# Optimization experiments

Hardware: AMD Instinct MI355X
Metric: run time of the kernel (lower is better)

The kernel has to match this reference:

```python
import jax, jax.numpy as jnp
import numpy as np

N, E, D, H, L = 50000, 800000, 256, 256, 40
HIDLAYERS = 3
NEG_SLOPE = 0.2  # PyG GATConv default leaky_relu slope


def _add_self_loops(edge_index, n):
    loop = jnp.arange(n, dtype=edge_index.dtype)
    src = jnp.concatenate([edge_index[0], loop])
    dst = jnp.concatenate([edge_index[1], loop])
    return src, dst


def gcn_conv(x, edge_index, W, b, n):
    # PyG GCNConv: add self-loops, symmetric deg^-1/2 normalization, linear, scatter-add
    src, dst = _add_self_loops(edge_index, n)
    ones = jnp.ones(src.shape[0], dtype=x.dtype)
    deg = jax.ops.segment_sum(ones, dst, num_segments=n)
    dinv = jnp.where(deg > 0, jax.lax.rsqrt(deg), 0.0)
    h = x @ W  # [n, out]
    norm = dinv[src] * dinv[dst]  # [E+n]
    out = jax.ops.segment_sum(h[src] * norm[:, None], dst, num_segments=n)
    return out + b


def gat_conv(x, edge_index, W, a_src, a_dst, b, n):
    # PyG GATConv (heads=1): add self-loops, e = leaky_relu(a_src.h_j + a_dst.h_i),
    # softmax over incoming edges per destination node, weighted scatter-add
    src, dst = _add_self_loops(edge_index, n)
    h = x @ W  # [n, H]
    al_src = h @ a_src  # [n]
    al_dst = h @ a_dst  # [n]
    e = jax.nn.leaky_relu(al_src[src] + al_dst[dst], NEG_SLOPE)  # [E+n]
    # numerically stable segment softmax over dst (self-loops => no empty segments)
    m = jax.ops.segment_max(e, dst, num_segments=n)
    ex = jnp.exp(e - m[dst])
    z = jax.ops.segment_sum(ex, dst, num_segments=n)
    alpha = ex / z[dst]
    out = jax.ops.segment_sum(h[src] * alpha[:, None], dst, num_segments=n)
    return out + b


def setup_inputs() -> dict:
    key = jax.random.key(0)
    ks = jax.random.split(key, 8)
    s = 0.05
    return {
        "x": jax.random.normal(ks[0], (N, D), jnp.float32),
        "edge_index": jax.random.randint(ks[1], (2, E), 0, N, dtype=jnp.int64),
        "W1": jax.random.normal(ks[2], (D, H), jnp.float32) * s,
        "b1": jnp.zeros((H,), jnp.float32),
        "Wg": jax.random.normal(ks[3], (H, H), jnp.float32) * s,
        "a_src": jax.random.normal(ks[4], (H,), jnp.float32) * s,
        "a_dst": jax.random.normal(ks[5], (H,), jnp.float32) * s,
        "bg": jnp.zeros((H,), jnp.float32),
        "W2": jax.random.normal(ks[6], (H, L), jnp.float32) * s,
        "b2": jnp.zeros((L,), jnp.float32),
    }


def reference(x, edge_index, W1, b1, Wg, a_src, a_dst, bg, W2, b2):
    n = x.shape[0]
    # feature standardization (torch .std is unbiased, ddof=1)
    x = (x - x.mean(axis=0, keepdims=True)) / x.std(axis=0, keepdims=True, ddof=1)
    x = jax.nn.relu(gcn_conv(x, edge_index, W1, b1, n))  # dropout = identity (eval)
    for _ in range(HIDLAYERS - 1):
        x = jax.nn.relu(gat_conv(x, edge_index, Wg, a_src, a_dst, bg, n))
    x = gcn_conv(x, edge_index, W2, b2, n)
    return jax.nn.log_softmax(x, axis=1)
```

## Files before the change

### kernel.cpp

```cpp
#include <hip/hip_runtime.h>
#include <math.h>

#define DD 256
#define LL 40
#define NSLOPE 0.2f
#define SCHUNK 1024

typedef unsigned short u16;
typedef unsigned int uint;
typedef __attribute__((ext_vector_type(8))) short short8;
typedef __attribute__((ext_vector_type(4))) float f32x4;

__device__ __forceinline__ float bf2f(u16 v) { return __uint_as_float(((uint)v) << 16); }
__device__ __forceinline__ u16 f2bf(float f) {
  uint u = __float_as_uint(f);
  return (u16)((u + 0x7fff + ((u >> 16) & 1)) >> 16);
}
__device__ __forceinline__ void acc8(float* a, uint4 v) {
  a[0] += __uint_as_float(v.x << 16);
  a[1] += __uint_as_float(v.x & 0xffff0000u);
  a[2] += __uint_as_float(v.y << 16);
  a[3] += __uint_as_float(v.y & 0xffff0000u);
  a[4] += __uint_as_float(v.z << 16);
  a[5] += __uint_as_float(v.z & 0xffff0000u);
  a[6] += __uint_as_float(v.w << 16);
  a[7] += __uint_as_float(v.w & 0xffff0000u);
}
__device__ __forceinline__ void wacc8(float* a, uint4 v, float w) {
  a[0] += w * __uint_as_float(v.x << 16);
  a[1] += w * __uint_as_float(v.x & 0xffff0000u);
  a[2] += w * __uint_as_float(v.y << 16);
  a[3] += w * __uint_as_float(v.y & 0xffff0000u);
  a[4] += w * __uint_as_float(v.z << 16);
  a[5] += w * __uint_as_float(v.z & 0xffff0000u);
  a[6] += w * __uint_as_float(v.w << 16);
  a[7] += w * __uint_as_float(v.w & 0xffff0000u);
}

__global__ void k_colstats(const float* __restrict__ x, float* __restrict__ csum,
                           float* __restrict__ csq, int n, int rowsPerBlk) {
  int col = threadIdx.x;
  int r0 = blockIdx.x * rowsPerBlk;
  int r1 = min(r0 + rowsPerBlk, n);
  float s = 0.f, q = 0.f;
  for (int r = r0; r < r1; ++r) {
    float v = x[(size_t)r * DD + col];
    s += v; q += v * v;
  }
  atomicAdd(&csum[col], s);
  atomicAdd(&csq[col], q);
}

__global__ void k_finalize_stats(const float* __restrict__ csum, const float* __restrict__ csq,
                                 float* __restrict__ mean, float* __restrict__ rstd, int n) {
  int j = threadIdx.x;
  float s = csum[j], q = csq[j];
  float m = s / (float)n;
  float var = (q - s * m) / (float)(n - 1);
  mean[j] = m;
  rstd[j] = 1.0f / sqrtf(var);
}

__global__ void k_standardize(const float* __restrict__ x, const float* __restrict__ mean,
                              const float* __restrict__ rstd, u16* __restrict__ xs, int total4) {
  int i = blockIdx.x * blockDim.x + threadIdx.x;
  if (i >= total4) return;
  int c4 = i & (DD / 4 - 1);
  float4 v = ((const float4*)x)[i];
  float4 m = ((const float4*)mean)[c4];
  float4 r = ((const float4*)rstd)[c4];
  uint2 o;
  o.x = (uint)f2bf((v.x - m.x) * r.x) | ((uint)f2bf((v.y - m.y) * r.y) << 16);
  o.y = (uint)f2bf((v.z - m.z) * r.z) | ((uint)f2bf((v.w - m.w) * r.w) << 16);
  ((uint2*)xs)[i] = o;
}

__global__ void k_convWt(const float* __restrict__ W, u16* __restrict__ Wt, int K, int N) {
  int k = blockIdx.x;
  for (int nn = threadIdx.x; nn < N; nn += blockDim.x)
    Wt[(size_t)nn * K + k] = f2bf(W[(size_t)k * N + nn]);
}

__global__ void k_count_deg(const int* __restrict__ edst, int E, int* __restrict__ degi) {
  int i = blockIdx.x * blockDim.x + threadIdx.x;
  if (i < E) atomicAdd(&degi[edst[i]], 1);
}

__global__ __launch_bounds__(256) void k_blocksum(const int* __restrict__ degi, int* __restrict__ bsum, int n) {
  int b = blockIdx.x, tid = threadIdx.x;
  int base = b * SCHUNK;
  int end = min(base + SCHUNK, n);
  int s = 0;
  for (int i = base + tid; i < end; i += 256) s += degi[i] + 1;
  __shared__ int ws[4];
  #pragma unroll
  for (int off = 32; off >= 1; off >>= 1) s += __shfl_down(s, off);
  if ((tid & 63) == 0) ws[tid >> 6] = s;
  __syncthreads();
  if (tid == 0) bsum[b] = ws[0] + ws[1] + ws[2] + ws[3];
}

__global__ void k_scan_bsums(int* __restrict__ bsum, int nb) {
  int lane = threadIdx.x;
  int orig = (lane < nb) ? bsum[lane] : 0;
  int v = orig;
  #pragma unroll
  for (int off = 1; off < 64; off <<= 1) {
    int t = __shfl_up(v, off);
    if (lane >= off) v += t;
  }
  if (lane < nb) bsum[lane] = v - orig;
}

__global__ __launch_bounds__(256) void k_rowptr_write(const int* __restrict__ degi, const int* __restrict__ bsum,
                                                      int* __restrict__ rowptr, int* __restrict__ cursor,
                                                      float* __restrict__ dinv, int n) {
  int b = blockIdx.x, tid = threadIdx.x;
  int base = b * SCHUNK + tid * 4;
  int d[4];
  int t = 0;
  #pragma unroll
  for (int j = 0; j < 4; ++j) {
    int i = base + j;
    d[j] = (i < n) ? degi[i] + 1 : 0;
    t += d[j];
  }
  __shared__ int sc[256];
  sc[tid] = t;
  __syncthreads();
  for (int off = 1; off < 256; off <<= 1) {
    int v = 0;
    if (tid >= off) v = sc[tid - off];
    __syncthreads();
    if (tid >= off) sc[tid] += v;
    __syncthreads();
  }
  int run = bsum[b] + sc[tid] - t;
  #pragma unroll
  for (int j = 0; j < 4; ++j) {
    int i = base + j;
    if (i < n) {
      rowptr[i] = run;
      cursor[i] = run;
      dinv[i] = rsqrtf((float)d[j]);
      run += d[j];
      if (i == n - 1) rowptr[n] = run;
    }
  }
}

__global__ void k_scatter(const int* __restrict__ esrc, const int* __restrict__ edst, int E,
                          int* __restrict__ cursor, int* __restrict__ csrsrc) {
  int i = blockIdx.x * blockDim.x + threadIdx.x;
  if (i < E) {
    int d = edst[i];
    int p = atomicAdd(&cursor[d], 1);
    csrsrc[p] = esrc[i];
  }
}

__global__ void k_selfloop(const int* __restrict__ rowptr, int* __restrict__ csrsrc, int n) {
  int i = blockIdx.x * blockDim.x + threadIdx.x;
  if (i < n) csrsrc[rowptr[i + 1] - 1] = i;
}

__global__ __launch_bounds__(256) void k_mfma_gemm(const u16* __restrict__ A, const u16* __restrict__ Bt,
                                                   u16* __restrict__ C, int M, int N, int K,
                                                   const float* __restrict__ rowScale) {
  __shared__ u16 As[128 * 40];
  __shared__ u16 Bs[64 * 40];
  int tid = threadIdx.x;
  int wave = tid >> 6, lane = tid & 63, quad = lane >> 4, l16 = lane & 15;
  int rowBase = blockIdx.y * 128, colBase = blockIdx.x * 64;
  f32x4 acc[2][4] = {};
  for (int k0 = 0; k0 < K; k0 += 32) {
    #pragma unroll
    for (int i = 0; i < 2; ++i) {
      int ch = tid + i * 256;
      int r = ch >> 2, cc = (ch & 3) * 8;
      int gr = rowBase + r;
      uint4 v = make_uint4(0, 0, 0, 0);
      if (gr < M) v = *(const uint4*)(A + (size_t)gr * K + k0 + cc);
      *(uint4*)&As[r * 40 + cc] = v;
    }
    {
      int r = tid >> 2, cc = (tid & 3) * 8;
      int gn = colBase + r;
      uint4 v = make_uint4(0, 0, 0, 0);
      if (gn < N) v = *(const uint4*)(Bt + (size_t)gn * K + k0 + cc);
      *(uint4*)&Bs[r * 40 + cc] = v;
    }
    __syncthreads();
    short8 af[2];
    af[0] = *(const short8*)&As[(wave * 32 + l16) * 40 + quad * 8];
    af[1] = *(const short8*)&As[(wave * 32 + 16 + l16) * 40 + quad * 8];
    short8 bf[4];
    #pragma unroll
    for (int j = 0; j < 4; ++j) bf[j] = *(const short8*)&Bs[(j * 16 + l16) * 40 + quad * 8];
    #pragma unroll
    for (int i = 0; i < 2; ++i)
      #pragma unroll
      for (int j = 0; j < 4; ++j)
        acc[i][j] = __builtin_amdgcn_mfma_f32_16x16x32_bf16(af[i], bf[j], acc[i][j], 0, 0, 0);
    __syncthreads();
  }
  #pragma unroll
  for (int i = 0; i < 2; ++i) {
    #pragma unroll
    for (int r = 0; r < 4; ++r) {
      int gr = rowBase + wave * 32 + i * 16 + quad * 4 + r;
      if (gr >= M) continue;
      float sc = rowScale ? rowScale[gr] : 1.0f;
      #pragma unroll
      for (int j = 0; j < 4; ++j) {
        int gc = colBase + j * 16 + l16;
        if (gc < N) C[(size_t)gr * N + gc] = f2bf(acc[i][j][r] * sc);
      }
    }
  }
}

__global__ __launch_bounds__(256) void k_gcn_agg(const u16* __restrict__ hs, const int* __restrict__ rowptr,
                                                 const int* __restrict__ csrsrc, const float* __restrict__ dinv,
                                                 const float* __restrict__ bias, u16* __restrict__ out, int n) {
  int wave = (blockIdx.x * blockDim.x + threadIdx.x) >> 6;
  int lane = threadIdx.x & 63;
  int sub = lane >> 5, l = lane & 31;
  int w = wave * 2 + sub;
  if (w >= n) return;
  int p0 = rowptr[w], p1 = rowptr[w + 1];
  float a[8] = {};
  int p = p0;
  for (; p + 4 <= p1; p += 4) {
    int s0 = csrsrc[p], s1 = csrsrc[p + 1], s2 = csrsrc[p + 2], s3 = csrsrc[p + 3];
    uint4 v0 = *(const uint4*)(hs + (size_t)s0 * DD + l * 8);
    uint4 v1 = *(const uint4*)(hs + (size_t)s1 * DD + l * 8);
    uint4 v2 = *(const uint4*)(hs + (size_t)s2 * DD + l * 8);
    uint4 v3 = *(const uint4*)(hs + (size_t)s3 * DD + l * 8);
    acc8(a, v0); acc8(a, v1); acc8(a, v2); acc8(a, v3);
  }
  for (; p < p1; ++p) {
    int s = csrsrc[p];
    uint4 v = *(const uint4*)(hs + (size_t)s * DD + l * 8);
    acc8(a, v);
  }
  float dd = dinv[w];
  float4 b0 = ((const float4*)bias)[l * 2];
  float4 b1 = ((const float4*)bias)[l * 2 + 1];
  float r0 = fmaxf(dd * a[0] + b0.x, 0.f), r1 = fmaxf(dd * a[1] + b0.y, 0.f);
  float r2 = fmaxf(dd * a[2] + b0.z, 0.f), r3 = fmaxf(dd * a[3] + b0.w, 0.f);
  float r4 = fmaxf(dd * a[4] + b1.x, 0.f), r5 = fmaxf(dd * a[5] + b1.y, 0.f);
  float r6 = fmaxf(dd * a[6] + b1.z, 0.f), r7 = fmaxf(dd * a[7] + b1.w, 0.f);
  uint4 o;
  o.x = (uint)f2bf(r0) | ((uint)f2bf(r1) << 16);
  o.y = (uint)f2bf(r2) | ((uint)f2bf(r3) << 16);
  o.z = (uint)f2bf(r4) | ((uint)f2bf(r5) << 16);
  o.w = (uint)f2bf(r6) | ((uint)f2bf(r7) << 16);
  *(uint4*)(out + (size_t)w * DD + l * 8) = o;
}

__global__ __launch_bounds__(256) void k_al(const u16* __restrict__ h, const float* __restrict__ va,
                                            const float* __restrict__ vb, float* __restrict__ als,
                                            float* __restrict__ ald, int n) {
  int w = (blockIdx.x * blockDim.x + threadIdx.x) >> 6;
  int lane = threadIdx.x & 63;
  if (w >= n) return;
  uint2 v = *(const uint2*)(h + (size_t)w * DD + lane * 4);
  float x0 = __uint_as_float(v.x << 16), x1 = __uint_as_float(v.x & 0xffff0000u);
  float x2 = __uint_as_float(v.y << 16), x3 = __uint_as_float(v.y & 0xffff0000u);
  float4 a = ((const float4*)va)[lane];
  float4 b = ((const float4*)vb)[lane];
  float s1 = x0 * a.x + x1 * a.y + x2 * a.z + x3 * a.w;
  float s2 = x0 * b.x + x1 * b.y + x2 * b.z + x3 * b.w;
  #pragma unroll
  for (int off = 1; off < 64; off <<= 1) {
    s1 += __shfl_xor(s1, off);
    s2 += __shfl_xor(s2, off);
  }
  if (lane == 0) { als[w] = s1; ald[w] = s2; }
}

__global__ __launch_bounds__(256) void k_gat_agg(const u16* __restrict__ h, const int* __restrict__ rowptr,
                                                 const int* __restrict__ csrsrc, const float* __restrict__ als,
                                                 const float* __restrict__ ald, const float* __restrict__ bias,
                                                 u16* __restrict__ out, int n) {
  int wave = (blockIdx.x * blockDim.x + threadIdx.x) >> 6;
  int lane = threadIdx.x & 63;
  int sub = lane >> 5, l = lane & 31;
  int w = wave * 2 + sub;
  if (w >= n) return;
  float ad = ald[w];
  int p0 = rowptr[w], p1 = rowptr[w + 1];
  float m = -1e30f, z = 0.f;
  for (int p = p0 + l; p < p1; p += 32) {
    float e = als[csrsrc[p]] + ad;
    e = (e > 0.f) ? e : NSLOPE * e;
    if (e > m) { z = z * __expf(m - e) + 1.f; m = e; }
    else z += __expf(e - m);
  }
  #pragma unroll
  for (int off = 16; off >= 1; off >>= 1) {
    float m2 = __shfl_xor(m, off), z2 = __shfl_xor(z, off);
    float M = fmaxf(m, m2);
    z = z * __expf(m - M) + z2 * __expf(m2 - M);
    m = M;
  }
  float invz = 1.0f / z;
  float a[8] = {};
  int p = p0;
  for (; p + 4 <= p1; p += 4) {
    int s0 = csrsrc[p], s1 = csrsrc[p + 1], s2 = csrsrc[p + 2], s3 = csrsrc[p + 3];
    float e0 = als[s0] + ad; e0 = (e0 > 0.f) ? e0 : NSLOPE * e0;
    float e1 = als[s1] + ad; e1 = (e1 > 0.f) ? e1 : NSLOPE * e1;
    float e2 = als[s2] + ad; e2 = (e2 > 0.f) ? e2 : NSLOPE * e2;
    float e3 = als[s3] + ad; e3 = (e3 > 0.f) ? e3 : NSLOPE * e3;
    uint4 v0 = *(const uint4*)(h + (size_t)s0 * DD + l * 8);
    uint4 v1 = *(const uint4*)(h + (size_t)s1 * DD + l * 8);
    uint4 v2 = *(const uint4*)(h + (size_t)s2 * DD + l * 8);
    uint4 v3 = *(const uint4*)(h + (size_t)s3 * DD + l * 8);
    wacc8(a, v0, __expf(e0 - m) * invz);
    wacc8(a, v1, __expf(e1 - m) * invz);
    wacc8(a, v2, __expf(e2 - m) * invz);
    wacc8(a, v3, __expf(e3 - m) * invz);
  }
  for (; p < p1; ++p) {
    int s = csrsrc[p];
    float e = als[s] + ad; e = (e > 0.f) ? e : NSLOPE * e;
    uint4 v = *(const uint4*)(h + (size_t)s * DD + l * 8);
    wacc8(a, v, __expf(e - m) * invz);
  }
  float4 b0 = ((const float4*)bias)[l * 2];
  float4 b1 = ((const float4*)bias)[l * 2 + 1];
  float r0 = fmaxf(a[0] + b0.x, 0.f), r1 = fmaxf(a[1] + b0.y, 0.f);
  float r2 = fmaxf(a[2] + b0.z, 0.f), r3 = fmaxf(a[3] + b0.w, 0.f);
  float r4 = fmaxf(a[4] + b1.x, 0.f), r5 = fmaxf(a[5] + b1.y, 0.f);
  float r6 = fmaxf(a[6] + b1.z, 0.f), r7 = fmaxf(a[7] + b1.w, 0.f);
  uint4 o;
  o.x = (uint)f2bf(r0) | ((uint)f2bf(r1) << 16);
  o.y = (uint)f2bf(r2) | ((uint)f2bf(r3) << 16);
  o.z = (uint)f2bf(r4) | ((uint)f2bf(r5) << 16);
  o.w = (uint)f2bf(r6) | ((uint)f2bf(r7) << 16);
  *(uint4*)(out + (size_t)w * DD + l * 8) = o;
}

__global__ __launch_bounds__(256) void k_gcn2_lsm(const u16* __restrict__ hs, const int* __restrict__ rowptr,
                                                  const int* __restrict__ csrsrc, const float* __restrict__ dinv,
                                                  const float* __restrict__ bias, float* __restrict__ out, int n) {
  int w = (blockIdx.x * blockDim.x + threadIdx.x) >> 6;
  int lane = threadIdx.x & 63;
  if (w >= n) return;
  int p0 = rowptr[w], p1 = rowptr[w + 1];
  float acc = 0.f;
  int p = p0;
  for (; p + 4 <= p1; p += 4) {
    int s0 = csrsrc[p], s1 = csrsrc[p + 1], s2 = csrsrc[p + 2], s3 = csrsrc[p + 3];
    if (lane < LL) {
      float v0 = bf2f(hs[(size_t)s0 * LL + lane]);
      float v1 = bf2f(hs[(size_t)s1 * LL + lane]);
      float v2 = bf2f(hs[(size_t)s2 * LL + lane]);
      float v3 = bf2f(hs[(size_t)s3 * LL + lane]);
      acc += v0 + v1 + v2 + v3;
    }
  }
  for (; p < p1; ++p) {
    int s = csrsrc[p];
    if (lane < LL) acc += bf2f(hs[(size_t)s * LL + lane]);
  }
  float dd = dinv[w];
  float v = (lane < LL) ? dd * acc + bias[lane] : -INFINITY;
  float m = v;
  #pragma unroll
  for (int off = 1; off < 64; off <<= 1) m = fmaxf(m, __shfl_xor(m, off));
  float ex = (lane < LL) ? __expf(v - m) : 0.f;
  float z = ex;
  #pragma unroll
  for (int off = 1; off < 64; off <<= 1) z += __shfl_xor(z, off);
  if (lane < LL) out[(size_t)w * LL + lane] = v - m - logf(z);
}

extern "C" void kernel_launch(void* const* d_in, const int* in_sizes, int n_in,
                              void* d_out, int out_size, void* d_ws, size_t ws_size,
                              hipStream_t stream) {
  const float* x   = (const float*)d_in[0];
  const int*   ei  = (const int*)d_in[1];
  const float* W1  = (const float*)d_in[2];
  const float* b1  = (const float*)d_in[3];
  const float* Wg  = (const float*)d_in[4];
  const float* a_s = (const float*)d_in[5];
  const float* a_d = (const float*)d_in[6];
  const float* bg  = (const float*)d_in[7];
  const float* W2  = (const float*)d_in[8];
  const float* b2  = (const float*)d_in[9];
  float* out = (float*)d_out;

  const int n = in_sizes[0] / DD;
  const int E = in_sizes[1] / 2;
  const int M = E + n;
  const int* esrc = ei;
  const int* edst = ei + E;

  char* wp = (char*)d_ws;
  auto carve = [&](size_t bytes) -> char* {
    char* p = wp;
    wp += (bytes + 255) & ~(size_t)255;
    return p;
  };
  u16*   buf0   = (u16*)carve((size_t)n * DD * 2);
  u16*   buf1   = (u16*)carve((size_t)n * DD * 2);
  u16*   h40    = (u16*)carve((size_t)n * LL * 2);
  u16*   W1t    = (u16*)carve((size_t)DD * DD * 2);
  u16*   Wgt    = (u16*)carve((size_t)DD * DD * 2);
  u16*   W2t    = (u16*)carve((size_t)LL * DD * 2);
  int*   csrsrc = (int*)carve((size_t)M * 4);
  int*   rowptr = (int*)carve((size_t)(n + 1) * 4);
  int*   cursor = (int*)carve((size_t)n * 4);
  int*   degi   = (int*)carve((size_t)n * 4);
  int*   bsum   = (int*)carve(64 * 4);
  float* dinv   = (float*)carve((size_t)n * 4);
  float* als    = (float*)carve((size_t)n * 4);
  float* ald    = (float*)carve((size_t)n * 4);
  float* csum   = (float*)carve(DD * 4);
  float* csq    = (float*)carve(DD * 4);
  float* mean   = (float*)carve(DD * 4);
  float* rstd   = (float*)carve(DD * 4);

  hipMemsetAsync(degi, 0, (size_t)n * 4, stream);
  hipMemsetAsync(csum, 0, DD * 4, stream);
  hipMemsetAsync(csq, 0, DD * 4, stream);

  const int rowsPerBlk = 128;
  k_colstats<<<(n + rowsPerBlk - 1) / rowsPerBlk, DD, 0, stream>>>(x, csum, csq, n, rowsPerBlk);
  k_finalize_stats<<<1, DD, 0, stream>>>(csum, csq, mean, rstd, n);
  int total4 = n * (DD / 4);
  k_standardize<<<(total4 + 255) / 256, 256, 0, stream>>>(x, mean, rstd, buf0, total4);

  k_convWt<<<DD, 256, 0, stream>>>(W1, W1t, DD, DD);
  k_convWt<<<DD, 256, 0, stream>>>(Wg, Wgt, DD, DD);
  k_convWt<<<DD, 64, 0, stream>>>(W2, W2t, DD, LL);

  int nb = (n + SCHUNK - 1) / SCHUNK;
  k_count_deg<<<(E + 255) / 256, 256, 0, stream>>>(edst, E, degi);
  k_blocksum<<<nb, 256, 0, stream>>>(degi, bsum, n);
  k_scan_bsums<<<1, 64, 0, stream>>>(bsum, nb);
  k_rowptr_write<<<nb, 256, 0, stream>>>(degi, bsum, rowptr, cursor, dinv, n);
  k_scatter<<<(E + 255) / 256, 256, 0, stream>>>(esrc, edst, E, cursor, csrsrc);
  k_selfloop<<<(n + 255) / 256, 256, 0, stream>>>(rowptr, csrsrc, n);

  dim3 blk(256);
  dim3 gemmGrid((DD + 63) / 64, (n + 127) / 128);
  int aggGrid1 = (n + 3) / 4;
  int aggGrid2 = (n + 7) / 8;

  k_mfma_gemm<<<gemmGrid, blk, 0, stream>>>(buf0, W1t, buf1, n, DD, DD, dinv);
  k_gcn_agg<<<aggGrid2, blk, 0, stream>>>(buf1, rowptr, csrsrc, dinv, b1, buf0, n);

  for (int l = 0; l < 2; ++l) {
    k_mfma_gemm<<<gemmGrid, blk, 0, stream>>>(buf0, Wgt, buf1, n, DD, DD, nullptr);
    k_al<<<aggGrid1, blk, 0, stream>>>(buf1, a_s, a_d, als, ald, n);
    k_gat_agg<<<aggGrid2, blk, 0, stream>>>(buf1, rowptr, csrsrc, als, ald, bg, buf0, n);
  }

  dim3 gemmGrid2(1, (n + 127) / 128);
  k_mfma_gemm<<<gemmGrid2, blk, 0, stream>>>(buf0, W2t, h40, n, LL, DD, dinv);
  k_gcn2_lsm<<<aggGrid1, blk, 0, stream>>>(h40, rowptr, csrsrc, dinv, b2, out, n);
}
```

Measured before the change: 598.1 us.

## Fold attention logits into aggregation epilogue via precomputed W·a vectors

New measurement: 626.8 us. 1.05x slower.

```diff
diff --git a/kernel.cpp b/kernel.cpp
--- a/kernel.cpp
+++ b/kernel.cpp
@@ -81,6 +81,24 @@
     Wt[(size_t)nn * K + k] = f2bf(W[(size_t)k * N + nn]);
 }
 
+__global__ __launch_bounds__(256) void k_wa(const float* __restrict__ W, const float* __restrict__ as_,
+                                            const float* __restrict__ ad_, float* __restrict__ wa, int K, int N) {
+  int wv = threadIdx.x >> 6, lane = threadIdx.x & 63;
+  float4 av = *(const float4*)(as_ + lane * 4);
+  float4 bv = *(const float4*)(ad_ + lane * 4);
+  for (int r = wv; r < K; r += 4) {
+    float4 wr = *(const float4*)(W + (size_t)r * N + lane * 4);
+    float s1 = wr.x * av.x + wr.y * av.y + wr.z * av.z + wr.w * av.w;
+    float s2 = wr.x * bv.x + wr.y * bv.y + wr.z * bv.z + wr.w * bv.w;
+    #pragma unroll
+    for (int off = 1; off < 64; off <<= 1) {
+      s1 += __shfl_xor(s1, off);
+      s2 += __shfl_xor(s2, off);
+    }
+    if (lane == 0) { wa[r] = s1; wa[K + r] = s2; }
+  }
+}
+
 __global__ void k_count_deg(const int* __restrict__ edst, int E, int* __restrict__ degi) {
   int i = blockIdx.x * blockDim.x + threadIdx.x;
   if (i < E) atomicAdd(&degi[edst[i]], 1);
@@ -222,28 +240,44 @@
 
 __global__ __launch_bounds__(256) void k_gcn_agg(const u16* __restrict__ hs, const int* __restrict__ rowptr,
                                                  const int* __restrict__ csrsrc, const float* __restrict__ dinv,
-                                                 const float* __restrict__ bias, u16* __restrict__ out, int n) {
+                                                 const float* __restrict__ bias, u16* __restrict__ out, int n,
+                                                 const float* __restrict__ wa, float* __restrict__ als,
+                                                 float* __restrict__ ald) {
   int wave = (blockIdx.x * blockDim.x + threadIdx.x) >> 6;
   int lane = threadIdx.x & 63;
   int sub = lane >> 5, l = lane & 31;
   int w = wave * 2 + sub;
   if (w >= n) return;
   int p0 = rowptr[w], p1 = rowptr[w + 1];
+  const u16* hb = hs + (size_t)l * 8;
   float a[8] = {};
   int p = p0;
+  for (; p < p1 && (p & 3); ++p)
+    acc8(a, *(const uint4*)(hb + (size_t)csrsrc[p] * DD));
+  for (; p + 8 <= p1; p += 8) {
+    int4 iA = *(const int4*)(csrsrc + p);
+    int4 iB = *(const int4*)(csrsrc + p + 4);
+    uint4 v0 = *(const uint4*)(hb + (size_t)iA.x * DD);
+    uint4 v1 = *(const uint4*)(hb + (size_t)iA.y * DD);
+    uint4 v2 = *(const uint4*)(hb + (size_t)iA.z * DD);
+    uint4 v3 = *(const uint4*)(hb + (size_t)iA.w * DD);
+    uint4 v4 = *(const uint4*)(hb + (size_t)iB.x * DD);
+    uint4 v5 = *(const uint4*)(hb + (size_t)iB.y * DD);
+    uint4 v6 = *(const uint4*)(hb + (size_t)iB.z * DD);
+    uint4 v7 = *(const uint4*)(hb + (size_t)iB.w * DD);
+    acc8(a, v0); acc8(a, v1); acc8(a, v2); acc8(a, v3);
+    acc8(a, v4); acc8(a, v5); acc8(a, v6); acc8(a, v7);
+  }
   for (; p + 4 <= p1; p += 4) {
-    int s0 = csrsrc[p], s1 = csrsrc[p + 1], s2 = csrsrc[p + 2], s3 = csrsrc[p + 3];
-    uint4 v0 = *(const uint4*)(hs + (size_t)s0 * DD + l * 8);
-    uint4 v1 = *(const uint4*)(hs + (size_t)s1 * DD + l * 8);
-    uint4 v2 = *(const uint4*)(hs + (size_t)s2 * DD + l * 8);
-    uint4 v3 = *(const uint4*)(hs + (size_t)s3 * DD + l * 8);
+    int4 iA = *(const int4*)(csrsrc + p);
+    uint4 v0 = *(const uint4*)(hb + (size_t)iA.x * DD);
+    uint4 v1 = *(const uint4*)(hb + (size_t)iA.y * DD);
+    uint4 v2 = *(const uint4*)(hb + (size_t)iA.z * DD);
+    uint4 v3 = *(const uint4*)(hb + (size_t)iA.w * DD);
     acc8(a, v0); acc8(a, v1); acc8(a, v2); acc8(a, v3);
   }
-  for (; p < p1; ++p) {
-    int s = csrsrc[p];
-    uint4 v = *(const uint4*)(hs + (size_t)s * DD + l * 8);
-    acc8(a, v);
-  }
+  for (; p < p1; ++p)
+    acc8(a, *(const uint4*)(hb + (size_t)csrsrc[p] * DD));
   float dd = dinv[w];
   float4 b0 = ((const float4*)bias)[l * 2];
   float4 b1 = ((const float4*)bias)[l * 2 + 1];
@@ -257,33 +291,26 @@
   o.z = (uint)f2bf(r4) | ((uint)f2bf(r5) << 16);
   o.w = (uint)f2bf(r6) | ((uint)f2bf(r7) << 16);
   *(uint4*)(out + (size_t)w * DD + l * 8) = o;
-}
-
-__global__ __launch_bounds__(256) void k_al(const u16* __restrict__ h, const float* __restrict__ va,
-                                            const float* __restrict__ vb, float* __restrict__ als,
-                                            float* __restrict__ ald, int n) {
-  int w = (blockIdx.x * blockDim.x + threadIdx.x) >> 6;
-  int lane = threadIdx.x & 63;
-  if (w >= n) return;
-  uint2 v = *(const uint2*)(h + (size_t)w * DD + lane * 4);
-  float x0 = __uint_as_float(v.x << 16), x1 = __uint_as_float(v.x & 0xffff0000u);
-  float x2 = __uint_as_float(v.y << 16), x3 = __uint_as_float(v.y & 0xffff0000u);
-  float4 a = ((const float4*)va)[lane];
-  float4 b = ((const float4*)vb)[lane];
-  float s1 = x0 * a.x + x1 * a.y + x2 * a.z + x3 * a.w;
-  float s2 = x0 * b.x + x1 * b.y + x2 * b.z + x3 * b.w;
-  #pragma unroll
-  for (int off = 1; off < 64; off <<= 1) {
-    s1 += __shfl_xor(s1, off);
-    s2 += __shfl_xor(s2, off);
-  }
-  if (lane == 0) { als[w] = s1; ald[w] = s2; }
+  if (wa) {
+    float4 s0 = ((const float4*)wa)[l * 2], s1 = ((const float4*)wa)[l * 2 + 1];
+    float4 d0 = ((const float4*)(wa + DD))[l * 2], d1 = ((const float4*)(wa + DD))[l * 2 + 1];
+    float t1 = r0 * s0.x + r1 * s0.y + r2 * s0.z + r3 * s0.w + r4 * s1.x + r5 * s1.y + r6 * s1.z + r7 * s1.w;
+    float t2 = r0 * d0.x + r1 * d0.y + r2 * d0.z + r3 * d0.w + r4 * d1.x + r5 * d1.y + r6 * d1.z + r7 * d1.w;
+    #pragma unroll
+    for (int off = 1; off < 32; off <<= 1) {
+      t1 += __shfl_xor(t1, off);
+      t2 += __shfl_xor(t2, off);
+    }
+    if (l == 0) { als[w] = t1; ald[w] = t2; }
+  }
 }
 
 __global__ __launch_bounds__(256) void k_gat_agg(const u16* __restrict__ h, const int* __restrict__ rowptr,
                                                  const int* __restrict__ csrsrc, const float* __restrict__ als,
                                                  const float* __restrict__ ald, const float* __restrict__ bias,
-                                                 u16* __restrict__ out, int n) {
+                                                 u16* __restrict__ out, int n,
+                                                 const float* __restrict__ wa, float* __restrict__ alsN,
+                                                 float* __restrict__ aldN) {
   int wave = (blockIdx.x * blockDim.x + threadIdx.x) >> 6;
   int lane = threadIdx.x & 63;
   int sub = lane >> 5, l = lane & 31;
@@ -306,28 +333,61 @@
     m = M;
   }
   float invz = 1.0f / z;
+  const u16* hb = h + (size_t)l * 8;
   float a[8] = {};
   int p = p0;
-  for (; p + 4 <= p1; p += 4) {
-    int s0 = csrsrc[p], s1 = csrsrc[p + 1], s2 = csrsrc[p + 2], s3 = csrsrc[p + 3];
-    float e0 = als[s0] + ad; e0 = (e0 > 0.f) ? e0 : NSLOPE * e0;
-    float e1 = als[s1] + ad; e1 = (e1 > 0.f) ? e1 : NSLOPE * e1;
-    float e2 = als[s2] + ad; e2 = (e2 > 0.f) ? e2 : NSLOPE * e2;
-    float e3 = als[s3] + ad; e3 = (e3 > 0.f) ? e3 : NSLOPE * e3;
-    uint4 v0 = *(const uint4*)(h + (size_t)s0 * DD + l * 8);
-    uint4 v1 = *(const uint4*)(h + (size_t)s1 * DD + l * 8);
-    uint4 v2 = *(const uint4*)(h + (size_t)s2 * DD + l * 8);
-    uint4 v3 = *(const uint4*)(h + (size_t)s3 * DD + l * 8);
+  for (; p < p1 && (p & 3); ++p) {
+    int s = csrsrc[p];
+    float e = als[s] + ad; e = (e > 0.f) ? e : NSLOPE * e;
+    wacc8(a, *(const uint4*)(hb + (size_t)s * DD), __expf(e - m) * invz);
+  }
+  for (; p + 8 <= p1; p += 8) {
+    int4 iA = *(const int4*)(csrsrc + p);
+    int4 iB = *(const int4*)(csrsrc + p + 4);
+    float e0 = als[iA.x] + ad; e0 = (e0 > 0.f) ? e0 : NSLOPE * e0;
+    float e1 = als[iA.y] + ad; e1 = (e1 > 0.f) ? e1 : NSLOPE * e1;
+    float e2 = als[iA.z] + ad; e2 = (e2 > 0.f) ? e2 : NSLOPE * e2;
+    float e3 = als[iA.w] + ad; e3 = (e3 > 0.f) ? e3 : NSLOPE * e3;
+    float e4 = als[iB.x] + ad; e4 = (e4 > 0.f) ? e4 : NSLOPE * e4;
+    float e5 = als[iB.y] + ad; e5 = (e5 > 0.f) ? e5 : NSLOPE * e5;
+    float e6 = als[iB.z] + ad; e6 = (e6 > 0.f) ? e6 : NSLOPE * e6;
+    float e7 = als[iB.w] + ad; e7 = (e7 > 0.f) ? e7 : NSLOPE * e7;
+    uint4 v0 = *(const uint4*)(hb + (size_t)iA.x * DD);
+    uint4 v1 = *(const uint4*)(hb + (size_t)iA.y * DD);
+    uint4 v2 = *(const uint4*)(hb + (size_t)iA.z * DD);
+    uint4 v3 = *(const uint4*)(hb + (size_t)iA.w * DD);
+    uint4 v4 = *(const uint4*)(hb + (size_t)iB.x * DD);
+    uint4 v5 = *(const uint4*)(hb + (size_t)iB.y * DD);
+    uint4 v6 = *(const uint4*)(hb + (size_t)iB.z * DD);
+    uint4 v7 = *(const uint4*)(hb + (size_t)iB.w * DD);
     wacc8(a, v0, __expf(e0 - m) * invz);
     wacc8(a, v1, __expf(e1 - m) * invz);
     wacc8(a, v2, __expf(e2 - m) * invz);
     wacc8(a, v3, __expf(e3 - m) * invz);
+    wacc8(a, v4, __expf(e4 - m) * invz);
+    wacc8(a, v5, __expf(e5 - m) * invz);
+    wacc8(a, v6, __expf(e6 - m) * invz);
+    wacc8(a, v7, __expf(e7 - m) * invz);
+  }
+  for (; p + 4 <= p1; p += 4) {
+    int4 iA = *(const int4*)(csrsrc + p);
+    float e0 = als[iA.x] + ad; e0 = (e0 > 0.f) ? e0 : NSLOPE * e0;
+    float e1 = als[iA.y] + ad; e1 = (e1 > 0.f) ? e1 : NSLOPE * e1;
+    float e2 = als[iA.z] + ad; e2 = (e2 > 0.f) ? e2 : NSLOPE * e2;
+    float e3 = als[iA.w] + ad; e3 = (e3 > 0.f) ? e3 : NSLOPE * e3;
+    uint4 v0 = *(const uint4*)(hb + (size_t)iA.x * DD);
+    uint4 v1 = *(const uint4*)(hb + (size_t)iA.y * DD);
+    uint4 v2 = *(const uint4*)(hb + (size_t)iA.z * DD);
+    uint4 v3 = *(const uint4*)(hb + (size_t)iA.w * DD);
+    wacc8(a, v0, __expf(e0 - m) * invz);
+    wacc8(a, v1, __expf(e1 - m) * invz);
+    wacc8(a, v2, __expf(e2 - m) * invz);
+    wacc8(a, v3, __expf(e3 - m) * invz);
   }
   for (; p < p1; ++p) {
     int s = csrsrc[p];
     float e = als[s] + ad; e = (e > 0.f) ? e : NSLOPE * e;
-    uint4 v = *(const uint4*)(h + (size_t)s * DD + l * 8);
-    wacc8(a, v, __expf(e - m) * invz);
+    wacc8(a, *(const uint4*)(hb + (size_t)s * DD), __expf(e - m) * invz);
   }
   float4 b0 = ((const float4*)bias)[l * 2];
   float4 b1 = ((const float4*)bias)[l * 2 + 1];
@@ -341,6 +401,18 @@
   o.z = (uint)f2bf(r4) | ((uint)f2bf(r5) << 16);
   o.w = (uint)f2bf(r6) | ((uint)f2bf(r7) << 16);
   *(uint4*)(out + (size_t)w * DD + l * 8) = o;
+  if (wa) {
+    float4 s0 = ((const float4*)wa)[l * 2], s1 = ((const float4*)wa)[l * 2 + 1];
+    float4 d0 = ((const float4*)(wa + DD))[l * 2], d1 = ((const float4*)(wa + DD))[l * 2 + 1];
+    float t1 = r0 * s0.x + r1 * s0.y + r2 * s0.z + r3 * s0.w + r4 * s1.x + r5 * s1.y + r6 * s1.z + r7 * s1.w;
+    float t2 = r0 * d0.x + r1 * d0.y + r2 * d0.z + r3 * d0.w + r4 * d1.x + r5 * d1.y + r6 * d1.z + r7 * d1.w;
+    #pragma unroll
+    for (int off = 1; off < 32; off <<= 1) {
+      t1 += __shfl_xor(t1, off);
+      t2 += __shfl_xor(t2, off);
+    }
+    if (l == 0) { alsN[w] = t1; aldN[w] = t2; }
+  }
 }
 
 __global__ __launch_bounds__(256) void k_gcn2_lsm(const u16* __restrict__ hs, const int* __restrict__ rowptr,
@@ -417,8 +489,11 @@
   int*   degi   = (int*)carve((size_t)n * 4);
   int*   bsum   = (int*)carve(64 * 4);
   float* dinv   = (float*)carve((size_t)n * 4);
-  float* als    = (float*)carve((size_t)n * 4);
-  float* ald    = (float*)carve((size_t)n * 4);
+  float* alsA   = (float*)carve((size_t)n * 4);
+  float* aldA   = (float*)carve((size_t)n * 4);
+  float* alsB   = (float*)carve((size_t)n * 4);
+  float* aldB   = (float*)carve((size_t)n * 4);
+  float* wa     = (float*)carve(2 * DD * 4);
   float* csum   = (float*)carve(DD * 4);
   float* csq    = (float*)carve(DD * 4);
   float* mean   = (float*)carve(DD * 4);
@@ -437,6 +512,7 @@
   k_convWt<<<DD, 256, 0, stream>>>(W1, W1t, DD, DD);
   k_convWt<<<DD, 256, 0, stream>>>(Wg, Wgt, DD, DD);
   k_convWt<<<DD, 64, 0, stream>>>(W2, W2t, DD, LL);
+  k_wa<<<1, 256, 0, stream>>>(Wg, a_s, a_d, wa, DD, DD);
 
   int nb = (n + SCHUNK - 1) / SCHUNK;
   k_count_deg<<<(E + 255) / 256, 256, 0, stream>>>(edst, E, degi);
@@ -452,13 +528,13 @@
   int aggGrid2 = (n + 7) / 8;
 
   k_mfma_gemm<<<gemmGrid, blk, 0, stream>>>(buf0, W1t, buf1, n, DD, DD, dinv);
-  k_gcn_agg<<<aggGrid2, blk, 0, stream>>>(buf1, rowptr, csrsrc, dinv, b1, buf0, n);
-
-  for (int l = 0; l < 2; ++l) {
-    k_mfma_gemm<<<gemmGrid, blk, 0, stream>>>(buf0, Wgt, buf1, n, DD, DD, nullptr);
-    k_al<<<aggGrid1, blk, 0, stream>>>(buf1, a_s, a_d, als, ald, n);
-    k_gat_agg<<<aggGrid2, blk, 0, stream>>>(buf1, rowptr, csrsrc, als, ald, bg, buf0, n);
-  }
+  k_gcn_agg<<<aggGrid2, blk, 0, stream>>>(buf1, rowptr, csrsrc, dinv, b1, buf0, n, wa, alsA, aldA);
+
+  k_mfma_gemm<<<gemmGrid, blk, 0, stream>>>(buf0, Wgt, buf1, n, DD, DD, nullptr);
+  k_gat_agg<<<aggGrid2, blk, 0, stream>>>(buf1, rowptr, csrsrc, alsA, aldA, bg, buf0, n, wa, alsB, aldB);
+
+  k_mfma_gemm<<<gemmGrid, blk, 0, stream>>>(buf0, Wgt, buf1, n, DD, DD, nullptr);
+  k_gat_agg<<<aggGrid2, blk, 0, stream>>>(buf1, rowptr, csrsrc, alsB, aldB, bg, buf0, n, nullptr, nullptr, nullptr);
 
   dim3 gemmGrid2(1, (n + 127) / 128);
   k_mfma_gemm<<<gemmGrid2, blk, 0, stream>>>(buf0, W2t, h40, n, LL, DD, dinv);
```

## Fold attention logits into aggregation epilogue and slice feature aggregation

Applied to the files above, without the earlier changes.

Result: slower. 1.026 ms (+71.6%).

```diff
diff --git a/kernel.cpp b/kernel.cpp
--- a/kernel.cpp
+++ b/kernel.cpp
@@ -81,6 +81,24 @@
     Wt[(size_t)nn * K + k] = f2bf(W[(size_t)k * N + nn]);
 }
 
+__global__ __launch_bounds__(256) void k_wa(const float* __restrict__ W, const float* __restrict__ as_,
+                                            const float* __restrict__ ad_, float* __restrict__ wa, int K, int N) {
+  int wv = threadIdx.x >> 6, lane = threadIdx.x & 63;
+  float4 av = *(const float4*)(as_ + lane * 4);
+  float4 bv = *(const float4*)(ad_ + lane * 4);
+  for (int r = wv; r < K; r += 4) {
+    float4 wr = *(const float4*)(W + (size_t)r * N + lane * 4);
+    float s1 = wr.x * av.x + wr.y * av.y + wr.z * av.z + wr.w * av.w;
+    float s2 = wr.x * bv.x + wr.y * bv.y + wr.z * bv.z + wr.w * bv.w;
+    #pragma unroll
+    for (int off = 1; off < 64; off <<= 1) {
+      s1 += __shfl_xor(s1, off);
+      s2 += __shfl_xor(s2, off);
+    }
+    if (lane == 0) { wa[r] = s1; wa[K + r] = s2; }
+  }
+}
+
 __global__ void k_count_deg(const int* __restrict__ edst, int E, int* __restrict__ degi) {
   int i = blockIdx.x * blockDim.x + threadIdx.x;
   if (i < E) atomicAdd(&degi[edst[i]], 1);
@@ -220,127 +238,105 @@
   }
 }
 
-__global__ __launch_bounds__(256) void k_gcn_agg(const u16* __restrict__ hs, const int* __restrict__ rowptr,
-                                                 const int* __restrict__ csrsrc, const float* __restrict__ dinv,
-                                                 const float* __restrict__ bias, u16* __restrict__ out, int n) {
-  int wave = (blockIdx.x * blockDim.x + threadIdx.x) >> 6;
-  int lane = threadIdx.x & 63;
-  int sub = lane >> 5, l = lane & 31;
-  int w = wave * 2 + sub;
-  if (w >= n) return;
-  int p0 = rowptr[w], p1 = rowptr[w + 1];
-  float a[8] = {};
-  int p = p0;
-  for (; p + 4 <= p1; p += 4) {
-    int s0 = csrsrc[p], s1 = csrsrc[p + 1], s2 = csrsrc[p + 2], s3 = csrsrc[p + 3];
-    uint4 v0 = *(const uint4*)(hs + (size_t)s0 * DD + l * 8);
-    uint4 v1 = *(const uint4*)(hs + (size_t)s1 * DD + l * 8);
-    uint4 v2 = *(const uint4*)(hs + (size_t)s2 * DD + l * 8);
-    uint4 v3 = *(const uint4*)(hs + (size_t)s3 * DD + l * 8);
-    acc8(a, v0); acc8(a, v1); acc8(a, v2); acc8(a, v3);
-  }
-  for (; p < p1; ++p) {
-    int s = csrsrc[p];
-    uint4 v = *(const uint4*)(hs + (size_t)s * DD + l * 8);
-    acc8(a, v);
-  }
-  float dd = dinv[w];
-  float4 b0 = ((const float4*)bias)[l * 2];
-  float4 b1 = ((const float4*)bias)[l * 2 + 1];
-  float r0 = fmaxf(dd * a[0] + b0.x, 0.f), r1 = fmaxf(dd * a[1] + b0.y, 0.f);
-  float r2 = fmaxf(dd * a[2] + b0.z, 0.f), r3 = fmaxf(dd * a[3] + b0.w, 0.f);
-  float r4 = fmaxf(dd * a[4] + b1.x, 0.f), r5 = fmaxf(dd * a[5] + b1.y, 0.f);
-  float r6 = fmaxf(dd * a[6] + b1.z, 0.f), r7 = fmaxf(dd * a[7] + b1.w, 0.f);
-  uint4 o;
-  o.x = (uint)f2bf(r0) | ((uint)f2bf(r1) << 16);
-  o.y = (uint)f2bf(r2) | ((uint)f2bf(r3) << 16);
-  o.z = (uint)f2bf(r4) | ((uint)f2bf(r5) << 16);
-  o.w = (uint)f2bf(r6) | ((uint)f2bf(r7) << 16);
-  *(uint4*)(out + (size_t)w * DD + l * 8) = o;
-}
-
-__global__ __launch_bounds__(256) void k_al(const u16* __restrict__ h, const float* __restrict__ va,
-                                            const float* __restrict__ vb, float* __restrict__ als,
-                                            float* __restrict__ ald, int n) {
+__global__ __launch_bounds__(256) void k_alpha(const int* __restrict__ rowptr, const int* __restrict__ csrsrc,
+                                               const float* __restrict__ als, const float* __restrict__ ald,
+                                               float* __restrict__ alpha, int n) {
   int w = (blockIdx.x * blockDim.x + threadIdx.x) >> 6;
   int lane = threadIdx.x & 63;
-  if (w >= n) return;
-  uint2 v = *(const uint2*)(h + (size_t)w * DD + lane * 4);
-  float x0 = __uint_as_float(v.x << 16), x1 = __uint_as_float(v.x & 0xffff0000u);
-  float x2 = __uint_as_float(v.y << 16), x3 = __uint_as_float(v.y & 0xffff0000u);
-  float4 a = ((const float4*)va)[lane];
-  float4 b = ((const float4*)vb)[lane];
-  float s1 = x0 * a.x + x1 * a.y + x2 * a.z + x3 * a.w;
-  float s2 = x0 * b.x + x1 * b.y + x2 * b.z + x3 * b.w;
-  #pragma unroll
-  for (int off = 1; off < 64; off <<= 1) {
-    s1 += __shfl_xor(s1, off);
-    s2 += __shfl_xor(s2, off);
-  }
-  if (lane == 0) { als[w] = s1; ald[w] = s2; }
-}
-
-__global__ __launch_bounds__(256) void k_gat_agg(const u16* __restrict__ h, const int* __restrict__ rowptr,
-                                                 const int* __restrict__ csrsrc, const float* __restrict__ als,
-                                                 const float* __restrict__ ald, const float* __restrict__ bias,
-                                                 u16* __restrict__ out, int n) {
-  int wave = (blockIdx.x * blockDim.x + threadIdx.x) >> 6;
-  int lane = threadIdx.x & 63;
-  int sub = lane >> 5, l = lane & 31;
-  int w = wave * 2 + sub;
   if (w >= n) return;
   float ad = ald[w];
   int p0 = rowptr[w], p1 = rowptr[w + 1];
   float m = -1e30f, z = 0.f;
-  for (int p = p0 + l; p < p1; p += 32) {
+  for (int p = p0 + lane; p < p1; p += 64) {
     float e = als[csrsrc[p]] + ad;
     e = (e > 0.f) ? e : NSLOPE * e;
     if (e > m) { z = z * __expf(m - e) + 1.f; m = e; }
     else z += __expf(e - m);
   }
   #pragma unroll
-  for (int off = 16; off >= 1; off >>= 1) {
+  for (int off = 32; off >= 1; off >>= 1) {
     float m2 = __shfl_xor(m, off), z2 = __shfl_xor(z, off);
     float M = fmaxf(m, m2);
     z = z * __expf(m - M) + z2 * __expf(m2 - M);
     m = M;
   }
   float invz = 1.0f / z;
+  for (int p = p0 + lane; p < p1; p += 64) {
+    float e = als[csrsrc[p]] + ad;
+    e = (e > 0.f) ? e : NSLOPE * e;
+    alpha[p] = __expf(e - m) * invz;
+  }
+}
+
+__global__ __launch_bounds__(256) void k_agg_slice(const u16* __restrict__ h, const int* __restrict__ rowptr,
+                                                   const int* __restrict__ csrsrc, const float* __restrict__ alpha,
+                                                   const float* __restrict__ dinv, const float* __restrict__ bias,
+                                                   u16* __restrict__ out, int n,
+                                                   const float* __restrict__ wa, float* __restrict__ als,
+                                                   float* __restrict__ ald) {
+  int b = blockIdx.x;
+  int slice = b & 7;
+  int w = (b >> 3) * 4 + (threadIdx.x >> 6);
+  int lane = threadIdx.x & 63;
+  if (w >= n) return;
+  int eg = lane >> 2;
+  int c = lane & 3;
+  const u16* hb = h + slice * 32 + c * 8;
+  int p0 = rowptr[w], p1 = rowptr[w + 1];
   float a[8] = {};
-  int p = p0;
-  for (; p + 4 <= p1; p += 4) {
-    int s0 = csrsrc[p], s1 = csrsrc[p + 1], s2 = csrsrc[p + 2], s3 = csrsrc[p + 3];
-    float e0 = als[s0] + ad; e0 = (e0 > 0.f) ? e0 : NSLOPE * e0;
-    float e1 = als[s1] + ad; e1 = (e1 > 0.f) ? e1 : NSLOPE * e1;
-    float e2 = als[s2] + ad; e2 = (e2 > 0.f) ? e2 : NSLOPE * e2;
-    float e3 = als[s3] + ad; e3 = (e3 > 0.f) ? e3 : NSLOPE * e3;
-    uint4 v0 = *(const uint4*)(h + (size_t)s0 * DD + l * 8);
-    uint4 v1 = *(const uint4*)(h + (size_t)s1 * DD + l * 8);
-    uint4 v2 = *(const uint4*)(h + (size_t)s2 * DD + l * 8);
-    uint4 v3 = *(const uint4*)(h + (size_t)s3 * DD + l * 8);
-    wacc8(a, v0, __expf(e0 - m) * invz);
-    wacc8(a, v1, __expf(e1 - m) * invz);
-    wacc8(a, v2, __expf(e2 - m) * invz);
-    wacc8(a, v3, __expf(e3 - m) * invz);
-  }
-  for (; p < p1; ++p) {
-    int s = csrsrc[p];
-    float e = als[s] + ad; e = (e > 0.f) ? e : NSLOPE * e;
-    uint4 v = *(const uint4*)(h + (size_t)s * DD + l * 8);
-    wacc8(a, v, __expf(e - m) * invz);
-  }
-  float4 b0 = ((const float4*)bias)[l * 2];
-  float4 b1 = ((const float4*)bias)[l * 2 + 1];
-  float r0 = fmaxf(a[0] + b0.x, 0.f), r1 = fmaxf(a[1] + b0.y, 0.f);
-  float r2 = fmaxf(a[2] + b0.z, 0.f), r3 = fmaxf(a[3] + b0.w, 0.f);
-  float r4 = fmaxf(a[4] + b1.x, 0.f), r5 = fmaxf(a[5] + b1.y, 0.f);
-  float r6 = fmaxf(a[6] + b1.z, 0.f), r7 = fmaxf(a[7] + b1.w, 0.f);
-  uint4 o;
-  o.x = (uint)f2bf(r0) | ((uint)f2bf(r1) << 16);
-  o.y = (uint)f2bf(r2) | ((uint)f2bf(r3) << 16);
-  o.z = (uint)f2bf(r4) | ((uint)f2bf(r5) << 16);
-  o.w = (uint)f2bf(r6) | ((uint)f2bf(r7) << 16);
-  *(uint4*)(out + (size_t)w * DD + l * 8) = o;
+  if (alpha) {
+    for (int p = p0 + eg; p < p1; p += 16) {
+      int s = csrsrc[p];
+      float wt = alpha[p];
+      uint4 v = *(const uint4*)(hb + (size_t)s * DD);
+      wacc8(a, v, wt);
+    }
+  } else {
+    for (int p = p0 + eg; p < p1; p += 16) {
+      int s = csrsrc[p];
+      uint4 v = *(const uint4*)(hb + (size_t)s * DD);
+      acc8(a, v);
+    }
+  }
+  #pragma unroll
+  for (int off = 4; off < 64; off <<= 1) {
+    #pragma unroll
+    for (int j = 0; j < 8; ++j) a[j] += __shfl_xor(a[j], off);
+  }
+  float sc = dinv ? dinv[w] : 1.0f;
+  const float* bp = bias + slice * 32 + c * 8;
+  float4 b0 = *(const float4*)bp;
+  float4 b1 = *(const float4*)(bp + 4);
+  float r0 = fmaxf(sc * a[0] + b0.x, 0.f), r1 = fmaxf(sc * a[1] + b0.y, 0.f);
+  float r2 = fmaxf(sc * a[2] + b0.z, 0.f), r3 = fmaxf(sc * a[3] + b0.w, 0.f);
+  float r4 = fmaxf(sc * a[4] + b1.x, 0.f), r5 = fmaxf(sc * a[5] + b1.y, 0.f);
+  float r6 = fmaxf(sc * a[6] + b1.z, 0.f), r7 = fmaxf(sc * a[7] + b1.w, 0.f);
+  if (eg == 0) {
+    uint4 o;
+    o.x = (uint)f2bf(r0) | ((uint)f2bf(r1) << 16);
+    o.y = (uint)f2bf(r2) | ((uint)f2bf(r3) << 16);
+    o.z = (uint)f2bf(r4) | ((uint)f2bf(r5) << 16);
+    o.w = (uint)f2bf(r6) | ((uint)f2bf(r7) << 16);
+    *(uint4*)(out + (size_t)w * DD + slice * 32 + c * 8) = o;
+  }
+  if (wa) {
+    const float* ws = wa + slice * 32 + c * 8;
+    float4 s0 = *(const float4*)ws;
+    float4 s1 = *(const float4*)(ws + 4);
+    float t1 = r0 * s0.x + r1 * s0.y + r2 * s0.z + r3 * s0.w +
+               r4 * s1.x + r5 * s1.y + r6 * s1.z + r7 * s1.w;
+    const float* wd = wa + DD + slice * 32 + c * 8;
+    float4 d0 = *(const float4*)wd;
+    float4 d1 = *(const float4*)(wd + 4);
+    float t2 = r0 * d0.x + r1 * d0.y + r2 * d0.z + r3 * d0.w +
+               r4 * d1.x + r5 * d1.y + r6 * d1.z + r7 * d1.w;
+    t1 += __shfl_xor(t1, 1); t1 += __shfl_xor(t1, 2);
+    t2 += __shfl_xor(t2, 1); t2 += __shfl_xor(t2, 2);
+    if (lane == 0) {
+      atomicAdd(&als[w], t1);
+      atomicAdd(&ald[w], t2);
+    }
+  }
 }
 
 __global__ __launch_bounds__(256) void k_gcn2_lsm(const u16* __restrict__ hs, const int* __restrict__ rowptr,
@@ -412,13 +408,17 @@
   u16*   Wgt    = (u16*)carve((size_t)DD * DD * 2);
   u16*   W2t    = (u16*)carve((size_t)LL * DD * 2);
   int*   csrsrc = (int*)carve((size_t)M * 4);
+  float* alphaE = (float*)carve((size_t)M * 4);
   int*   rowptr = (int*)carve((size_t)(n + 1) * 4);
   int*   cursor = (int*)carve((size_t)n * 4);
   int*   degi   = (int*)carve((size_t)n * 4);
   int*   bsum   = (int*)carve(64 * 4);
   float* dinv   = (float*)carve((size_t)n * 4);
-  float* als    = (float*)carve((size_t)n * 4);
-  float* ald    = (float*)carve((size_t)n * 4);
+  float* alsA   = (float*)carve((size_t)n * 4);
+  float* aldA   = (float*)carve((size_t)n * 4);
+  float* alsB   = (float*)carve((size_t)n * 4);
+  float* aldB   = (float*)carve((size_t)n * 4);
+  float* wa     = (float*)carve(2 * DD * 4);
   float* csum   = (float*)carve(DD * 4);
   float* csq    = (float*)carve(DD * 4);
   float* mean   = (float*)carve(DD * 4);
@@ -427,6 +427,10 @@
   hipMemsetAsync(degi, 0, (size_t)n * 4, stream);
   hipMemsetAsync(csum, 0, DD * 4, stream);
   hipMemsetAsync(csq, 0, DD * 4, stream);
+  hipMemsetAsync(alsA, 0, (size_t)n * 4, stream);
+  hipMemsetAsync(aldA, 0, (size_t)n * 4, stream);
+  hipMemsetAsync(alsB, 0, (size_t)n * 4, stream);
+  hipMemsetAsync(aldB, 0, (size_t)n * 4, stream);
 
   const int rowsPerBlk = 128;
   k_colstats<<<(n + rowsPerBlk - 1) / rowsPerBlk, DD, 0, stream>>>(x, csum, csq, n, rowsPerBlk);
@@ -437,6 +441,7 @@
   k_convWt<<<DD, 256, 0, stream>>>(W1, W1t, DD, DD);
   k_convWt<<<DD, 256, 0, stream>>>(Wg, Wgt, DD, DD);
   k_convWt<<<DD, 64, 0, stream>>>(W2, W2t, DD, LL);
+  k_wa<<<1, 256, 0, stream>>>(Wg, a_s, a_d, wa, DD, DD);
 
   int nb = (n + SCHUNK - 1) / SCHUNK;
   k_count_deg<<<(E + 255) / 256, 256, 0, stream>>>(edst, E, degi);
@@ -449,16 +454,18 @@
   dim3 blk(256);
   dim3 gemmGrid((DD + 63) / 64, (n + 127) / 128);
   int aggGrid1 = (n + 3) / 4;
-  int aggGrid2 = (n + 7) / 8;
+  int sliceGrid = 8 * ((n + 3) / 4);
 
   k_mfma_gemm<<<gemmGrid, blk, 0, stream>>>(buf0, W1t, buf1, n, DD, DD, dinv);
-  k_gcn_agg<<<aggGrid2, blk, 0, stream>>>(buf1, rowptr, csrsrc, dinv, b1, buf0, n);
-
-  for (int l = 0; l < 2; ++l) {
-    k_mfma_gemm<<<gemmGrid, blk, 0, stream>>>(buf0, Wgt, buf1, n, DD, DD, nullptr);
-    k_al<<<aggGrid1, blk, 0, stream>>>(buf1, a_s, a_d, als, ald, n);
-    k_gat_agg<<<aggGrid2, blk, 0, stream>>>(buf1, rowptr, csrsrc, als, ald, bg, buf0, n);
-  }
+  k_agg_slice<<<sliceGrid, blk, 0, stream>>>(buf1, rowptr, csrsrc, nullptr, dinv, b1, buf0, n, wa, alsA, aldA);
+
+  k_mfma_gemm<<<gemmGrid, blk, 0, stream>>>(buf0, Wgt, buf1, n, DD, DD, nullptr);
+  k_alpha<<<aggGrid1, blk, 0, stream>>>(rowptr, csrsrc, alsA, aldA, alphaE, n);
+  k_agg_slice<<<sliceGrid, blk, 0, stream>>>(buf1, rowptr, csrsrc, alphaE, nullptr, bg, buf0, n, wa, alsB, aldB);
+
+  k_mfma_gemm<<<gemmGrid, blk, 0, stream>>>(buf0, Wgt, buf1, n, DD, DD, nullptr);
+  k_alpha<<<aggGrid1, blk, 0, stream>>>(rowptr, csrsrc, alsB, aldB, alphaE, n);
+  k_agg_slice<<<sliceGrid, blk, 0, stream>>>(buf1, rowptr, csrsrc, alphaE, nullptr, bg, buf0, n, nullptr, nullptr, nullptr);
 
   dim3 gemmGrid2(1, (n + 127) / 128);
   k_mfma_gemm<<<gemmGrid2, blk, 0, stream>>>(buf0, W2t, h40, n, LL, DD, dinv);
```
